# Kernel tuning notes

Measured on AMD Instinct MI355X. Metric: run time of the kernel, lower is better.

The kernel has to match this reference:

```python
import jax, jax.numpy as jnp
import numpy as np

BN_EPS = 1e-5
N_NODES = 100000
N_EDGES = 300000
IN_FEAT = 256
HIDDEN = 128
N_ETYPES = 4


def setup_inputs() -> dict:
    key = jax.random.key(0)
    ks = jax.random.split(key, 10)
    s = 1.0 / np.sqrt(2 * IN_FEAT)
    return {
        "h_src": jax.random.normal(ks[0], (N_NODES, IN_FEAT), jnp.float32),
        "h_dst": jax.random.normal(ks[1], (N_NODES, IN_FEAT), jnp.float32),
        "src_nodes": jax.random.randint(ks[2], (N_EDGES,), 0, N_NODES),
        "dst_nodes": jax.random.randint(ks[3], (N_EDGES,), 0, N_NODES),
        "etype_idx": 0,
        "W1": jax.random.normal(ks[4], (2 * IN_FEAT, HIDDEN), jnp.float32) * s,
        "b1": jnp.zeros((HIDDEN,), jnp.float32),
        "bn_gamma": jnp.ones((HIDDEN,), jnp.float32),
        "bn_beta": jnp.zeros((HIDDEN,), jnp.float32),
        "bn_mean": jnp.zeros((HIDDEN,), jnp.float32),
        "bn_var": jnp.ones((HIDDEN,), jnp.float32),
        "emb": jax.random.normal(ks[5], (N_ETYPES, HIDDEN), jnp.float32),
        "W2": jax.random.normal(ks[6], (HIDDEN, HIDDEN // 2), jnp.float32) * (1.0 / np.sqrt(HIDDEN)),
        "b2": jnp.zeros((HIDDEN // 2,), jnp.float32),
        "W3": jax.random.normal(ks[7], (HIDDEN // 2, 1), jnp.float32) * (1.0 / np.sqrt(HIDDEN // 2)),
        "b3": jnp.zeros((1,), jnp.float32),
    }


def reference(h_src, h_dst, src_nodes, dst_nodes, etype_idx,
              W1, b1, bn_gamma, bn_beta, bn_mean, bn_var,
              emb, W2, b2, W3, b3):
    # gather endpoint features and concat -> [E, 2*in_feat]
    src_feat = h_src[src_nodes]
    dst_feat = h_dst[dst_nodes]
    edge_feat = jnp.concatenate([src_feat, dst_feat], axis=1)
    # Linear + ReLU (Dropout is identity in eval) + BatchNorm1d (running stats)
    x = jax.nn.relu(edge_feat @ W1 + b1)
    x = (x - bn_mean) * jax.lax.rsqrt(bn_var + BN_EPS) * bn_gamma + bn_beta
    # add edge-type embedding (broadcast over edges)
    x = x + emb[etype_idx]
    # per-edge-type predictor MLP -> scalar score per edge
    x = jax.nn.relu(x @ W2 + b2)
    scores = (x @ W3 + b3).squeeze(-1)
    return scores
```

## Files before the change

kernel.cpp:

```cpp
#include <hip/hip_runtime.h>
#include <hip/hip_bf16.h>


typedef __attribute__((ext_vector_type(8))) short bf16x8;
typedef __attribute__((ext_vector_type(4))) float f32x4;

constexpr int HID   = 128;
constexpr int ETILE = 64;
constexpr int AS    = 72;
constexpr int XS    = 136;

__device__ inline ushort f2bf(float f) {
    union { __hip_bfloat16 h; ushort u; } cv;
    cv.h = __float2bfloat16(f);
    return cv.u;
}

__global__ __launch_bounds__(256)
void prep_kernel(const float* __restrict__ W1, const float* __restrict__ W2,
                 const float* __restrict__ bn_gamma, const float* __restrict__ bn_beta,
                 const float* __restrict__ bn_mean, const float* __restrict__ bn_var,
                 const float* __restrict__ emb, const int* __restrict__ etype,
                 ushort* __restrict__ B1p, ushort* __restrict__ B2p,
                 float* __restrict__ sc, float* __restrict__ sh)
{
    int i = blockIdx.x * blockDim.x + threadIdx.x;
    if (i < 65536) {
        int j = i & 7, lane = (i >> 3) & 63, ct = (i >> 9) & 7, ks = i >> 12;
        int k = ks * 32 + (lane >> 4) * 8 + j;
        int c = ct * 16 + (lane & 15);
        B1p[i] = f2bf(W1[k * HID + c]);
    } else if (i < 65536 + 8192) {
        int p = i - 65536;
        int j = p & 7, lane = (p >> 3) & 63, ct = (p >> 9) & 3, ks = p >> 11;
        int k = ks * 32 + (lane >> 4) * 8 + j;
        int c = ct * 16 + (lane & 15);
        B2p[p] = f2bf(W2[k * 64 + c]);
    } else if (i < 65536 + 8192 + HID) {
        int c = i - 65536 - 8192;
        float s = bn_gamma[c] * rsqrtf(bn_var[c] + 1e-5f);
        sc[c] = s;
        sh[c] = bn_beta[c] - bn_mean[c] * s + emb[etype[0] * HID + c];
    }
}

__global__ __launch_bounds__(256, 4)
void edge_mlp_mfma(const float* __restrict__ h_src, const float* __restrict__ h_dst,
                   const int* __restrict__ src_nodes, const int* __restrict__ dst_nodes,
                   const ushort* __restrict__ B1p, const ushort* __restrict__ B2p,
                   const float* __restrict__ b1, const float* __restrict__ sc,
                   const float* __restrict__ sh, const float* __restrict__ b2,
                   const float* __restrict__ W3, const float* __restrict__ b3,
                   float* __restrict__ out, int n_edges)
{
    __shared__ ushort sA[2][ETILE * AS];
    __shared__ int s_src[ETILE], s_dst[ETILE];

    const int t    = threadIdx.x;
    const int lane = t & 63;
    const int w    = t >> 6;
    const int lr   = lane & 15;
    const int lq   = lane >> 4;
    const int ebase = blockIdx.x * ETILE;

    if (t < ETILE) {
        int e = ebase + t;
        s_src[t] = src_nodes[e < n_edges ? e : 0];
    } else if (t < 2 * ETILE) {
        int e = ebase + t - ETILE;
        s_dst[t - ETILE] = dst_nodes[e < n_edges ? e : 0];
    }

    f32x4 acc[4][2];
#pragma unroll
    for (int rt = 0; rt < 4; ++rt)
#pragma unroll
        for (int c = 0; c < 2; ++c) acc[rt][c] = (f32x4)0.0f;

    float4 rA[4], rB[4];
    bf16x8 Bf0[4], Bf1[4];

#define PHASE_BAR() do {                                                       \
        asm volatile("s_waitcnt lgkmcnt(0)" ::: "memory");                     \
        __builtin_amdgcn_s_barrier();                                          \
    } while (0)

#define LOADC(kc, R) do {                                                      \
        const float* hp = ((kc) < 4) ? h_src : h_dst;                          \
        const int* sidx = ((kc) < 4) ? s_src : s_dst;                          \
        const int koff = ((kc) & 3) * 64;                                      \
        _Pragma("unroll")                                                      \
        for (int i = 0; i < 4; ++i) {                                          \
            int f = t + i * 256; int e = f >> 4; int q = f & 15;               \
            R[i] = *reinterpret_cast<const float4*>(                           \
                hp + (size_t)sidx[e] * 256 + koff + q * 4);                    \
        } } while (0)

#define BLOAD(kc, BR) do {                                                     \
        _Pragma("unroll")                                                      \
        for (int s = 0; s < 2; ++s)                                            \
        _Pragma("unroll")                                                      \
        for (int c = 0; c < 2; ++c)                                            \
            BR[s * 2 + c] = *reinterpret_cast<const bf16x8*>(                  \
                B1p + (size_t)((((kc) * 2 + s) * 8 + 2 * w + c) * 64 + lane) * 8); \
        } while (0)

#define STOREC(B, R) do {                                                      \
        _Pragma("unroll")                                                      \
        for (int i = 0; i < 4; ++i) {                                          \
            int f = t + i * 256; int e = f >> 4; int q = f & 15;               \
            ushort4 bv;                                                        \
            bv.x = f2bf(R[i].x); bv.y = f2bf(R[i].y);                          \
            bv.z = f2bf(R[i].z); bv.w = f2bf(R[i].w);                          \
            *reinterpret_cast<ushort4*>(&sA[B][e * AS + q * 4]) = bv;          \
        } } while (0)

#define COMP(B, BR) do {                                                       \
        _Pragma("unroll")                                                      \
        for (int ks = 0; ks < 2; ++ks) {                                       \
            _Pragma("unroll")                                                  \
            for (int rt = 0; rt < 4; ++rt) {                                   \
                bf16x8 af = *reinterpret_cast<const bf16x8*>(                  \
                    &sA[B][(rt * 16 + lr) * AS + ks * 32 + lq * 8]);           \
                acc[rt][0] = __builtin_amdgcn_mfma_f32_16x16x32_bf16(af, BR[ks * 2 + 0], acc[rt][0], 0, 0, 0); \
                acc[rt][1] = __builtin_amdgcn_mfma_f32_16x16x32_bf16(af, BR[ks * 2 + 1], acc[rt][1], 0, 0, 0); \
            } } } while (0)

    __syncthreads();

    LOADC(0, rA);
    BLOAD(0, Bf0);
    STOREC(0, rA);
    LOADC(1, rB);
    BLOAD(1, Bf1);
    PHASE_BAR();

    LOADC(2, rA);  COMP(0, Bf0);  BLOAD(2, Bf0);  STOREC(1, rB);  PHASE_BAR();
    LOADC(3, rB);  COMP(1, Bf1);  BLOAD(3, Bf1);  STOREC(0, rA);  PHASE_BAR();
    LOADC(4, rA);  COMP(0, Bf0);  BLOAD(4, Bf0);  STOREC(1, rB);  PHASE_BAR();
    LOADC(5, rB);  COMP(1, Bf1);  BLOAD(5, Bf1);  STOREC(0, rA);  PHASE_BAR();
    LOADC(6, rA);  COMP(0, Bf0);  BLOAD(6, Bf0);  STOREC(1, rB);  PHASE_BAR();
    LOADC(7, rB);  COMP(1, Bf1);  BLOAD(7, Bf1);  STOREC(0, rA);  PHASE_BAR();
                   COMP(0, Bf0);                  STOREC(1, rB);  PHASE_BAR();
                   COMP(1, Bf1);

#undef LOADC
#undef BLOAD
#undef STOREC
#undef COMP
#undef PHASE_BAR

    __syncthreads();
    ushort* sX = &sA[0][0];
#pragma unroll
    for (int ctl = 0; ctl < 2; ++ctl) {
        int c = (2 * w + ctl) * 16 + lr;
        float bb = b1[c], s = sc[c], z = sh[c];
#pragma unroll
        for (int rt = 0; rt < 4; ++rt)
#pragma unroll
            for (int r = 0; r < 4; ++r) {
                float x = fmaxf(acc[rt][ctl][r] + bb, 0.0f);
                sX[(rt * 16 + lq * 4 + r) * XS + c] = f2bf(fmaf(x, s, z));
            }
    }
    __syncthreads();

    f32x4 acc2[4];
#pragma unroll
    for (int ct = 0; ct < 4; ++ct) acc2[ct] = (f32x4)0.0f;

#pragma unroll
    for (int ks = 0; ks < 4; ++ks) {
        bf16x8 af = *reinterpret_cast<const bf16x8*>(
            &sX[(w * 16 + lr) * XS + ks * 32 + lq * 8]);
#pragma unroll
        for (int ct = 0; ct < 4; ++ct) {
            bf16x8 bf = *reinterpret_cast<const bf16x8*>(
                B2p + (size_t)((ks * 4 + ct) * 64 + lane) * 8);
            acc2[ct] = __builtin_amdgcn_mfma_f32_16x16x32_bf16(af, bf, acc2[ct], 0, 0, 0);
        }
    }

    float w3v[4], b2v[4];
#pragma unroll
    for (int ct = 0; ct < 4; ++ct) {
        int c = ct * 16 + lr;
        w3v[ct] = W3[c];
        b2v[ct] = b2[c];
    }
#pragma unroll
    for (int r = 0; r < 4; ++r) {
        float sum = 0.0f;
#pragma unroll
        for (int ct = 0; ct < 4; ++ct)
            sum += fmaxf(acc2[ct][r] + b2v[ct], 0.0f) * w3v[ct];
        sum += __shfl_xor(sum, 1);
        sum += __shfl_xor(sum, 2);
        sum += __shfl_xor(sum, 4);
        sum += __shfl_xor(sum, 8);
        int e = ebase + w * 16 + lq * 4 + r;
        if (lr == 0 && e < n_edges) out[e] = sum + b3[0];
    }
}

extern "C" void kernel_launch(void* const* d_in, const int* in_sizes, int n_in,
                              void* d_out, int out_size, void* d_ws, size_t ws_size,
                              hipStream_t stream) {
    const float* h_src     = (const float*)d_in[0];
    const float* h_dst     = (const float*)d_in[1];
    const int*   src_nodes = (const int*)d_in[2];
    const int*   dst_nodes = (const int*)d_in[3];
    const int*   etype     = (const int*)d_in[4];
    const float* W1        = (const float*)d_in[5];
    const float* b1        = (const float*)d_in[6];
    const float* bn_gamma  = (const float*)d_in[7];
    const float* bn_beta   = (const float*)d_in[8];
    const float* bn_mean   = (const float*)d_in[9];
    const float* bn_var    = (const float*)d_in[10];
    const float* emb       = (const float*)d_in[11];
    const float* W2        = (const float*)d_in[12];
    const float* b2        = (const float*)d_in[13];
    const float* W3        = (const float*)d_in[14];
    const float* b3        = (const float*)d_in[15];

    ushort* B1p = (ushort*)d_ws;
    ushort* B2p = B1p + 65536;
    float*  scp = (float*)(B2p + 8192);
    float*  shp = scp + HID;

    prep_kernel<<<(65536 + 8192 + HID + 255) / 256, 256, 0, stream>>>(
        W1, W2, bn_gamma, bn_beta, bn_mean, bn_var, emb, etype, B1p, B2p, scp, shp);

    const int n_edges = in_sizes[2];
    const int grid = (n_edges + ETILE - 1) / ETILE;
    edge_mlp_mfma<<<grid, 256, 0, stream>>>(h_src, h_dst, src_nodes, dst_nodes,
                                            B1p, B2p, b1, scp, shp, b2, W3, b3,
                                            (float*)d_out, n_edges);
}
```

Before: 97.02 us.

## Project node features through W1 before the edge gather

```diff
diff --git a/kernel.cpp b/kernel.cpp
--- a/kernel.cpp
+++ b/kernel.cpp
@@ -4,6 +4,7 @@
 
 typedef __attribute__((ext_vector_type(8))) short bf16x8;
 typedef __attribute__((ext_vector_type(4))) float f32x4;
+typedef __attribute__((ext_vector_type(8))) unsigned short u16x8;
 
 constexpr int HID   = 128;
 constexpr int ETILE = 64;
@@ -14,6 +15,9 @@
     union { __hip_bfloat16 h; ushort u; } cv;
     cv.h = __float2bfloat16(f);
     return cv.u;
+}
+__device__ inline float bf2f(ushort u) {
+    return __uint_as_float(((unsigned int)u) << 16);
 }
 
 __global__ __launch_bounds__(256)
@@ -44,6 +48,173 @@
     }
 }
 
+__global__ __launch_bounds__(256)
+void proj_kernel(const float* __restrict__ h_src, const float* __restrict__ h_dst,
+                 const ushort* __restrict__ B1p,
+                 ushort* __restrict__ Psrc, ushort* __restrict__ Pdst,
+                 int n_nodes, int ntiles)
+{
+    __shared__ ushort sX[ETILE * XS];
+
+    const int b    = blockIdx.x;
+    const int half = (b >= ntiles) ? 1 : 0;
+    const float* hp = half ? h_dst : h_src;
+    ushort* Pp      = half ? Pdst : Psrc;
+    const int nb   = (b - half * ntiles) * 64;
+
+    const int t    = threadIdx.x;
+    const int lane = t & 63;
+    const int w    = t >> 6;
+    const int lr   = lane & 15;
+    const int lq   = lane >> 4;
+
+    f32x4 acc[4][2];
+#pragma unroll
+    for (int rt = 0; rt < 4; ++rt)
+#pragma unroll
+        for (int c = 0; c < 2; ++c) acc[rt][c] = (f32x4)0.0f;
+
+#pragma unroll
+    for (int ksl = 0; ksl < 8; ++ksl) {
+        const int kstep = half * 8 + ksl;
+        bf16x8 bf0 = *reinterpret_cast<const bf16x8*>(
+            B1p + (size_t)((kstep * 8 + 2 * w) * 64 + lane) * 8);
+        bf16x8 bf1 = *reinterpret_cast<const bf16x8*>(
+            B1p + (size_t)((kstep * 8 + 2 * w + 1) * 64 + lane) * 8);
+#pragma unroll
+        for (int rt = 0; rt < 4; ++rt) {
+            int row = nb + rt * 16 + lr;
+            if (row >= n_nodes) row = n_nodes - 1;
+            const float* ap = hp + (size_t)row * 256 + ksl * 32 + lq * 8;
+            float4 a0 = *reinterpret_cast<const float4*>(ap);
+            float4 a1 = *reinterpret_cast<const float4*>(ap + 4);
+            bf16x8 af;
+            af[0] = (short)f2bf(a0.x); af[1] = (short)f2bf(a0.y);
+            af[2] = (short)f2bf(a0.z); af[3] = (short)f2bf(a0.w);
+            af[4] = (short)f2bf(a1.x); af[5] = (short)f2bf(a1.y);
+            af[6] = (short)f2bf(a1.z); af[7] = (short)f2bf(a1.w);
+            acc[rt][0] = __builtin_amdgcn_mfma_f32_16x16x32_bf16(af, bf0, acc[rt][0], 0, 0, 0);
+            acc[rt][1] = __builtin_amdgcn_mfma_f32_16x16x32_bf16(af, bf1, acc[rt][1], 0, 0, 0);
+        }
+    }
+
+#pragma unroll
+    for (int ctl = 0; ctl < 2; ++ctl) {
+        int c = (2 * w + ctl) * 16 + lr;
+#pragma unroll
+        for (int rt = 0; rt < 4; ++rt)
+#pragma unroll
+            for (int r = 0; r < 4; ++r)
+                sX[(rt * 16 + lq * 4 + r) * XS + c] = f2bf(acc[rt][ctl][r]);
+    }
+    __syncthreads();
+
+#pragma unroll
+    for (int i = 0; i < 4; ++i) {
+        int f = t + i * 256;
+        int e = f >> 4, q = f & 15;
+        if (nb + e < n_nodes) {
+            u16x8 v = *reinterpret_cast<const u16x8*>(&sX[e * XS + q * 8]);
+            *reinterpret_cast<u16x8*>(Pp + (size_t)(nb + e) * 128 + q * 8) = v;
+        }
+    }
+}
+
+__global__ __launch_bounds__(256)
+void edge_kernel(const ushort* __restrict__ Psrc, const ushort* __restrict__ Pdst,
+                 const int* __restrict__ src_nodes, const int* __restrict__ dst_nodes,
+                 const float* __restrict__ b1, const float* __restrict__ sc,
+                 const float* __restrict__ sh, const float* __restrict__ b2,
+                 const float* __restrict__ W3, const float* __restrict__ b3,
+                 const ushort* __restrict__ B2p, float* __restrict__ out, int n_edges)
+{
+    __shared__ ushort sX[ETILE * XS];
+    __shared__ int s_s[ETILE], s_d[ETILE];
+
+    const int t     = threadIdx.x;
+    const int lane  = t & 63;
+    const int w     = t >> 6;
+    const int lr    = lane & 15;
+    const int lq    = lane >> 4;
+    const int ebase = blockIdx.x * ETILE;
+
+    if (t < ETILE) {
+        int e = ebase + t;
+        s_s[t] = src_nodes[e < n_edges ? e : (n_edges - 1)];
+    } else if (t < 2 * ETILE) {
+        int e = ebase + t - ETILE;
+        s_d[t - ETILE] = dst_nodes[e < n_edges ? e : (n_edges - 1)];
+    }
+    __syncthreads();
+
+    {
+        const int e = t >> 2, q = t & 3;
+        const ushort* ps = Psrc + (size_t)s_s[e] * 128 + q * 32;
+        const ushort* pd = Pdst + (size_t)s_d[e] * 128 + q * 32;
+#pragma unroll
+        for (int j = 0; j < 4; ++j) {
+            u16x8 a = *reinterpret_cast<const u16x8*>(ps + j * 8);
+            u16x8 b = *reinterpret_cast<const u16x8*>(pd + j * 8);
+            const int c0 = q * 32 + j * 8;
+            float4 b1a = *reinterpret_cast<const float4*>(b1 + c0);
+            float4 b1b = *reinterpret_cast<const float4*>(b1 + c0 + 4);
+            float4 sca = *reinterpret_cast<const float4*>(sc + c0);
+            float4 scb = *reinterpret_cast<const float4*>(sc + c0 + 4);
+            float4 sha = *reinterpret_cast<const float4*>(sh + c0);
+            float4 shb = *reinterpret_cast<const float4*>(sh + c0 + 4);
+            float bb[8] = {b1a.x, b1a.y, b1a.z, b1a.w, b1b.x, b1b.y, b1b.z, b1b.w};
+            float ss[8] = {sca.x, sca.y, sca.z, sca.w, scb.x, scb.y, scb.z, scb.w};
+            float zz[8] = {sha.x, sha.y, sha.z, sha.w, shb.x, shb.y, shb.z, shb.w};
+            u16x8 xo;
+#pragma unroll
+            for (int i = 0; i < 8; ++i) {
+                float v = bf2f((ushort)a[i]) + bf2f((ushort)b[i]) + bb[i];
+                v = fmaxf(v, 0.0f);
+                xo[i] = f2bf(fmaf(v, ss[i], zz[i]));
+            }
+            *reinterpret_cast<u16x8*>(&sX[e * XS + c0]) = xo;
+        }
+    }
+    __syncthreads();
+
+    f32x4 acc2[4];
+#pragma unroll
+    for (int ct = 0; ct < 4; ++ct) acc2[ct] = (f32x4)0.0f;
+
+#pragma unroll
+    for (int ks = 0; ks < 4; ++ks) {
+        bf16x8 af = *reinterpret_cast<const bf16x8*>(
+            &sX[(w * 16 + lr) * XS + ks * 32 + lq * 8]);
+#pragma unroll
+        for (int ct = 0; ct < 4; ++ct) {
+            bf16x8 bf = *reinterpret_cast<const bf16x8*>(
+                B2p + (size_t)((ks * 4 + ct) * 64 + lane) * 8);
+            acc2[ct] = __builtin_amdgcn_mfma_f32_16x16x32_bf16(af, bf, acc2[ct], 0, 0, 0);
+        }
+    }
+
+    float w3v[4], b2v[4];
+#pragma unroll
+    for (int ct = 0; ct < 4; ++ct) {
+        int c = ct * 16 + lr;
+        w3v[ct] = W3[c];
+        b2v[ct] = b2[c];
+    }
+#pragma unroll
+    for (int r = 0; r < 4; ++r) {
+        float sum = 0.0f;
+#pragma unroll
+        for (int ct = 0; ct < 4; ++ct)
+            sum += fmaxf(acc2[ct][r] + b2v[ct], 0.0f) * w3v[ct];
+        sum += __shfl_xor(sum, 1);
+        sum += __shfl_xor(sum, 2);
+        sum += __shfl_xor(sum, 4);
+        sum += __shfl_xor(sum, 8);
+        int e = ebase + w * 16 + lq * 4 + r;
+        if (lr == 0 && e < n_edges) out[e] = sum + b3[0];
+    }
+}
+
 __global__ __launch_bounds__(256, 4)
 void edge_mlp_mfma(const float* __restrict__ h_src, const float* __restrict__ h_dst,
                    const int* __restrict__ src_nodes, const int* __restrict__ dst_nodes,
@@ -224,17 +395,33 @@
     const float* W3        = (const float*)d_in[14];
     const float* b3        = (const float*)d_in[15];
 
+    const int n_edges = in_sizes[2];
+    const int n_nodes = in_sizes[0] / 256;
+
     ushort* B1p = (ushort*)d_ws;
     ushort* B2p = B1p + 65536;
     float*  scp = (float*)(B2p + 8192);
     float*  shp = scp + HID;
+    const size_t wbytes = (size_t)(65536 + 8192) * 2 + 256 * 4;
+    const size_t pbytes = (size_t)n_nodes * HID * 2;
+    ushort* Psrc = (ushort*)((char*)d_ws + wbytes);
+    ushort* Pdst = Psrc + (size_t)n_nodes * HID;
 
     prep_kernel<<<(65536 + 8192 + HID + 255) / 256, 256, 0, stream>>>(
         W1, W2, bn_gamma, bn_beta, bn_mean, bn_var, emb, etype, B1p, B2p, scp, shp);
 
-    const int n_edges = in_sizes[2];
-    const int grid = (n_edges + ETILE - 1) / ETILE;
-    edge_mlp_mfma<<<grid, 256, 0, stream>>>(h_src, h_dst, src_nodes, dst_nodes,
-                                            B1p, B2p, b1, scp, shp, b2, W3, b3,
-                                            (float*)d_out, n_edges);
-}
+    const int egrid = (n_edges + ETILE - 1) / ETILE;
+
+    if (ws_size >= wbytes + 2 * pbytes) {
+        const int ntiles = (n_nodes + 63) / 64;
+        proj_kernel<<<2 * ntiles, 256, 0, stream>>>(h_src, h_dst, B1p,
+                                                    Psrc, Pdst, n_nodes, ntiles);
+        edge_kernel<<<egrid, 256, 0, stream>>>(Psrc, Pdst, src_nodes, dst_nodes,
+                                               b1, scp, shp, b2, W3, b3, B2p,
+                                               (float*)d_out, n_edges);
+    } else {
+        edge_mlp_mfma<<<egrid, 256, 0, stream>>>(h_src, h_dst, src_nodes, dst_nodes,
+                                                 B1p, B2p, b1, scp, shp, b2, W3, b3,
+                                                 (float*)d_out, n_edges);
+    }
+}
```

Result: slower. 184.5 us (+90.2%).
